# Optimization experiments

Measured on AMD Instinct MI355X. Metric: run time of the kernel, lower is better.

## Reference

```python
import jax, jax.numpy as jnp
import numpy as np

N_EMBD = 1024
N_HEAD = 16
HEAD_SIZE = 64


def setup_inputs() -> dict:
    key = jax.random.key(0)
    ks = jax.random.split(key, 6)
    B, T, C, H, D = 2, 2048, N_EMBD, N_HEAD, HEAD_SIZE
    s = 1.0 / np.sqrt(C)
    x = jax.random.normal(ks[0], (B, T, C), dtype=jnp.float32)
    Wq = jax.random.normal(ks[1], (H, C, D), dtype=jnp.float32) * s
    Wk = jax.random.normal(ks[2], (H, C, D), dtype=jnp.float32) * s
    Wv = jax.random.normal(ks[3], (H, C, D), dtype=jnp.float32) * s
    Wo = jax.random.normal(ks[4], (H * D, C), dtype=jnp.float32) * (1.0 / np.sqrt(H * D))
    bo = jax.random.normal(ks[5], (C,), dtype=jnp.float32) * 0.01
    return {"x": x, "Wq": Wq, "Wk": Wk, "Wv": Wv, "Wo": Wo, "bo": bo}


def reference(x, Wq, Wk, Wv, Wo, bo):
    B, T, C = x.shape
    H, _, D = Wq.shape
    # Per-head projections, batched across heads: [B,H,T,D]
    q = jnp.einsum('btc,hcd->bhtd', x, Wq)
    k = jnp.einsum('btc,hcd->bhtd', x, Wk)
    v = jnp.einsum('btc,hcd->bhtd', x, Wv)
    # NOTE: original scales by sqrt(C) = sqrt(n_embd), not sqrt(head_size)
    scale = 1.0 / jnp.sqrt(jnp.float32(C))
    att = jnp.einsum('bhtd,bhsd->bhts', q, k) * scale  # [B,H,T,T]
    causal = jnp.tril(jnp.ones((T, T), dtype=bool))
    att = jnp.where(causal, att, -jnp.inf)
    att = jax.nn.softmax(att, axis=-1)
    # dropout omitted (eval mode / deterministic reference)
    out = jnp.einsum('bhts,bhsd->bhtd', att, v)  # [B,H,T,D]
    out = out.transpose(0, 2, 1, 3).reshape(B, T, H * D)
    return out @ Wo + bo
```

## Files before the change

kernel.cpp:

```cpp
#include <hip/hip_runtime.h>
#include <hip/hip_bf16.h>


typedef __hip_bfloat16 bf16;
typedef __bf16 v8bf __attribute__((ext_vector_type(8)));
typedef float  v4f  __attribute__((ext_vector_type(4)));
typedef unsigned long long u64;
typedef unsigned int u32;

#define MFMA16(a, b, c) __builtin_amdgcn_mfma_f32_16x16x32_bf16((a), (b), (c), 0, 0, 0)

__device__ __forceinline__ bf16 f2b(float x) { return __float2bfloat16(x); }
__device__ __forceinline__ __bf16 f2braw(float x) {
  bf16 t = __float2bfloat16(x);
  return *reinterpret_cast<__bf16*>(&t);
}
__device__ __forceinline__ unsigned short f2bu(float x) {
  bf16 t = __float2bfloat16(x);
  return *reinterpret_cast<unsigned short*>(&t);
}

__device__ __forceinline__ void load16_lds(const bf16* gptr, const bf16* lptr) {
  __builtin_amdgcn_global_load_lds(
      (const __attribute__((address_space(1))) u32*)gptr,
      (__attribute__((address_space(3))) u32*)lptr, 16, 0, 0);
}

__global__ __launch_bounds__(256) void prep_kernel(
    const float* __restrict__ x,
    const float* __restrict__ Wq, const float* __restrict__ Wk,
    const float* __restrict__ Wv, const float* __restrict__ Wo,
    bf16* __restrict__ xb, bf16* __restrict__ wt, bf16* __restrict__ wot)
{
  __shared__ float Lt[32][33];
  const int bid = blockIdx.x, tid = threadIdx.x;

  if (bid < 2048) {
    size_t i = ((size_t)bid * 256 + tid) * 8;
    float4 f0 = *(const float4*)(x + i);
    float4 f1 = *(const float4*)(x + i + 4);
    v8bf v;
    v[0] = f2braw(f0.x); v[1] = f2braw(f0.y); v[2] = f2braw(f0.z); v[3] = f2braw(f0.w);
    v[4] = f2braw(f1.x); v[5] = f2braw(f1.y); v[6] = f2braw(f1.z); v[7] = f2braw(f1.w);
    *(v8bf*)(xb + i) = v;
    return;
  }
  const int tx = tid & 31, ty = tid >> 5;
  if (bid < 5120) {
    const int idx = bid - 2048;
    const int z = idx >> 6, rem = idx & 63;
    const int p = z >> 4, h = z & 15;
    const float* ib = ((p == 0) ? Wq : (p == 1) ? Wk : Wv) + (size_t)h * 65536;
    bf16* ob = wt + (size_t)z * 65536;
    const int j0 = (rem & 1) * 32, i0 = (rem >> 1) * 32;
    #pragma unroll
    for (int r = 0; r < 4; ++r)
      Lt[ty + 8 * r][tx] = ib[(size_t)(i0 + ty + 8 * r) * 64 + j0 + tx];
    __syncthreads();
    #pragma unroll
    for (int r = 0; r < 4; ++r)
      ob[(size_t)(j0 + ty + 8 * r) * 1024 + i0 + tx] = f2b(Lt[tx][ty + 8 * r]);
  } else {
    const int idx = bid - 5120;
    const int j0 = (idx & 31) * 32, i0 = (idx >> 5) * 32;
    #pragma unroll
    for (int r = 0; r < 4; ++r)
      Lt[ty + 8 * r][tx] = Wo[(size_t)(i0 + ty + 8 * r) * 1024 + j0 + tx];
    __syncthreads();
    #pragma unroll
    for (int r = 0; r < 4; ++r)
      wot[(size_t)(j0 + ty + 8 * r) * 1024 + i0 + tx] = f2b(Lt[tx][ty + 8 * r]);
  }
}

__global__ __launch_bounds__(512, 2) void qkv_gemm_kernel(
    const bf16* __restrict__ xb, const bf16* __restrict__ wt,
    bf16* __restrict__ qkv)
{
  __shared__ __align__(16) bf16 Ash[2][256][64];
  __shared__ __align__(16) bf16 Bsh[2][192][64];

  const int mt = blockIdx.x, nt = blockIdx.y;
  const int tid = threadIdx.x, wid = tid >> 6, lane = tid & 63;
  const int ln = lane & 15, quad = lane >> 4;
  const int wm = wid >> 1, wn = wid & 1;
  const int m0 = mt * 256, n0 = nt * 192;

  const v4f vzero = {0.f, 0.f, 0.f, 0.f};
  v4f acc[4][6];
  #pragma unroll
  for (int mf = 0; mf < 4; ++mf)
    #pragma unroll
    for (int nf = 0; nf < 6; ++nf) acc[mf][nf] = vzero;

  const int r8 = lane >> 3, slot = (lane & 7) ^ r8;
  const bf16* gA0 = xb + (size_t)(m0 + (wid * 4 + 0) * 8 + r8) * 1024 + slot * 8;
  const bf16* gA1 = xb + (size_t)(m0 + (wid * 4 + 1) * 8 + r8) * 1024 + slot * 8;
  const bf16* gA2 = xb + (size_t)(m0 + (wid * 4 + 2) * 8 + r8) * 1024 + slot * 8;
  const bf16* gA3 = xb + (size_t)(m0 + (wid * 4 + 3) * 8 + r8) * 1024 + slot * 8;
  const bf16* gB0 = wt + (size_t)(n0 + (wid * 3 + 0) * 8 + r8) * 1024 + slot * 8;
  const bf16* gB1 = wt + (size_t)(n0 + (wid * 3 + 1) * 8 + r8) * 1024 + slot * 8;
  const bf16* gB2 = wt + (size_t)(n0 + (wid * 3 + 2) * 8 + r8) * 1024 + slot * 8;

  const int sw = ln & 7;
  const int fs0 = ((quad    ) ^ sw) * 8;
  const int fs1 = ((quad + 4) ^ sw) * 8;
  const int arow = (wm * 64 + ln) * 64;
  const int brow = (wn * 96 + ln) * 64;

  #define STAGE_A(BUF) {                                         \
    load16_lds(gA0, &Ash[BUF][(wid * 4 + 0) * 8][0]);            \
    load16_lds(gA1, &Ash[BUF][(wid * 4 + 1) * 8][0]);            \
    load16_lds(gA2, &Ash[BUF][(wid * 4 + 2) * 8][0]);            \
    load16_lds(gA3, &Ash[BUF][(wid * 4 + 3) * 8][0]);            \
    gA0 += 64; gA1 += 64; gA2 += 64; gA3 += 64; }
  #define STAGE_B(BUF) {                                         \
    load16_lds(gB0, &Bsh[BUF][(wid * 3 + 0) * 8][0]);            \
    load16_lds(gB1, &Bsh[BUF][(wid * 3 + 1) * 8][0]);            \
    load16_lds(gB2, &Bsh[BUF][(wid * 3 + 2) * 8][0]);            \
    gB0 += 64; gB1 += 64; gB2 += 64; }

  #define PHASE_SYNC() {                                         \
    __builtin_amdgcn_s_barrier();                                \
    asm volatile("s_waitcnt lgkmcnt(0)" ::: "memory");           \
    __builtin_amdgcn_sched_barrier(0); }

  #define QTILE(BUF, DOSTAGE, DOBOUND)                                     \
  {                                                                        \
    const bf16* aB = &Ash[BUF][0][0];                                      \
    const bf16* bB = &Bsh[BUF][0][0];                                      \
    v8bf af[4], bv[3];                                                     \
                              \
    _Pragma("unroll")                                                      \
    for (int mf = 0; mf < 4; ++mf)                                         \
      af[mf] = *(const v8bf*)(aB + arow + mf * 1024 + fs0);                \
    _Pragma("unroll")                                                      \
    for (int nf = 0; nf < 3; ++nf)                                         \
      bv[nf] = *(const v8bf*)(bB + brow + nf * 1024 + fs0);                \
    if (DOSTAGE) STAGE_A(BUF ^ 1)                                          \
    PHASE_SYNC()                                                           \
    __builtin_amdgcn_s_setprio(1);                                         \
    _Pragma("unroll")                                                      \
    for (int mf = 0; mf < 4; ++mf)                                         \
      _Pragma("unroll")                                                    \
      for (int nf = 0; nf < 3; ++nf)                                       \
        acc[mf][nf] = MFMA16(af[mf], bv[nf], acc[mf][nf]);                 \
    __builtin_amdgcn_s_setprio(0);                                         \
                                        \
    _Pragma("unroll")                                                      \
    for (int nf = 0; nf < 3; ++nf)                                         \
      bv[nf] = *(const v8bf*)(bB + brow + (nf + 3) * 1024 + fs0);          \
    if (DOSTAGE) STAGE_B(BUF ^ 1)                                          \
    PHASE_SYNC()                                                           \
    __builtin_amdgcn_s_setprio(1);                                         \
    _Pragma("unroll")                                                      \
    for (int mf = 0; mf < 4; ++mf)                                         \
      _Pragma("unroll")                                                    \
      for (int nf = 0; nf < 3; ++nf)                                       \
        acc[mf][nf + 3] = MFMA16(af[mf], bv[nf], acc[mf][nf + 3]);         \
    __builtin_amdgcn_s_setprio(0);                                         \
                                            \
    _Pragma("unroll")                                                      \
    for (int mf = 0; mf < 4; ++mf)                                         \
      af[mf] = *(const v8bf*)(aB + arow + mf * 1024 + fs1);                \
    _Pragma("unroll")                                                      \
    for (int nf = 0; nf < 3; ++nf)                                         \
      bv[nf] = *(const v8bf*)(bB + brow + nf * 1024 + fs1);                \
    PHASE_SYNC()                                                           \
    __builtin_amdgcn_s_setprio(1);                                         \
    _Pragma("unroll")                                                      \
    for (int mf = 0; mf < 4; ++mf)                                         \
      _Pragma("unroll")                                                    \
      for (int nf = 0; nf < 3; ++nf)                                       \
        acc[mf][nf] = MFMA16(af[mf], bv[nf], acc[mf][nf]);                 \
    __builtin_amdgcn_s_setprio(0);                                         \
                                                      \
    _Pragma("unroll")                                                      \
    for (int nf = 0; nf < 3; ++nf)                                         \
      bv[nf] = *(const v8bf*)(bB + brow + (nf + 3) * 1024 + fs1);          \
    PHASE_SYNC()                                                           \
    __builtin_amdgcn_s_setprio(1);                                         \
    _Pragma("unroll")                                                      \
    for (int mf = 0; mf < 4; ++mf)                                         \
      _Pragma("unroll")                                                    \
      for (int nf = 0; nf < 3; ++nf)                                       \
        acc[mf][nf + 3] = MFMA16(af[mf], bv[nf], acc[mf][nf + 3]);         \
    __builtin_amdgcn_s_setprio(0);                                         \
        \
    if (DOBOUND) {                                                         \
      asm volatile("s_waitcnt vmcnt(0) lgkmcnt(0)" ::: "memory");          \
      __builtin_amdgcn_s_barrier();                                        \
      __builtin_amdgcn_sched_barrier(0);                                   \
    }                                                                      \
  }

  STAGE_A(0)
  STAGE_B(0)
  asm volatile("s_waitcnt vmcnt(0)" ::: "memory");
  __builtin_amdgcn_s_barrier();
  __builtin_amdgcn_sched_barrier(0);

  #pragma unroll 1
  for (int it = 0; it < 7; ++it) {
    QTILE(0, 1, 1)
    QTILE(1, 1, 1)
  }
  QTILE(0, 1, 1)
  QTILE(1, 0, 0)
  #undef QTILE
  #undef PHASE_SYNC
  #undef STAGE_A
  #undef STAGE_B

  #pragma unroll
  for (int nf = 0; nf < 6; ++nf) {
    const int j = n0 + wn * 96 + nf * 16 + ln;
    const int p = j >> 10;
    const int h = (j >> 6) & 15;
    const int d = j & 63;
    if (p < 2) {
      const float scale = (p == 0) ? 0.0450841149f : 1.0f;
      bf16* base = qkv + (size_t)p * 4194304 + (size_t)h * 262144;
      #pragma unroll
      for (int mf = 0; mf < 4; ++mf)
        #pragma unroll
        for (int r = 0; r < 4; ++r) {
          int m = m0 + wm * 64 + mf * 16 + quad * 4 + r;
          base[(size_t)m * 64 + d] = f2b(acc[mf][nf][r] * scale);
        }
    } else {
      bf16* vb = qkv + (size_t)2 * 4194304 + (size_t)h * 262144;
      #pragma unroll
      for (int mf = 0; mf < 4; ++mf) {
        int mrow = m0 + wm * 64 + mf * 16 + quad * 4;
        int bi = mrow >> 11, t0 = mrow & 2047;
        u64 pk = (u64)f2bu(acc[mf][nf][0]) |
                 ((u64)f2bu(acc[mf][nf][1]) << 16) |
                 ((u64)f2bu(acc[mf][nf][2]) << 32) |
                 ((u64)f2bu(acc[mf][nf][3]) << 48);
        *(u64*)(vb + (size_t)bi * 131072 + (size_t)d * 2048 + t0) = pk;
      }
    }
  }
}

__global__ __launch_bounds__(256, 4) void attn_kernel(
    const bf16* __restrict__ qkv, bf16* __restrict__ att)
{
  union ShU {
    struct { bf16 K[2][64][64]; bf16 V[2][64][64]; } t;
    struct { float O[2][64][36]; float L[2][36]; } c;
  };
  __shared__ __align__(16) ShU sh;

  const int fid = blockIdx.x;
  const int j = fid >> 5;
  const int jr = j & 7, jq = j >> 3;
  const int mt = (jq == 0) ? (31 - jr) : (jq == 1) ? (8 + jr)
               : (jq == 2) ? (23 - jr) : jr;
  const int grp = fid & 31;
  const int b = grp >> 4, h = grp & 15;

  const int tid = threadIdx.x, w = tid >> 6, lane = tid & 63;
  const int ln = lane & 15, quad = lane >> 4;
  const int qh = w & 1, kh = w >> 1;

  const bf16* qbase  = qkv + (size_t)h * 262144 + (size_t)b * 131072;
  const bf16* kbase  = qbase + 4194304;
  const bf16* vtbase = qbase + 8388608;

  const int l8 = lane & 7, r8 = lane >> 3;
  const int slot = l8 ^ r8;
  const int p0 = w * 16 + r8, p1 = p0 + 8;
  const int kp0 = (p0 & 32) | ((p0 & 12) << 1) | ((p0 & 16) >> 2) | (p0 & 3);
  const int kp1 = (p1 & 32) | ((p1 & 12) << 1) | ((p1 & 16) >> 2) | (p1 & 3);
  const bf16* gkp0 = kbase + kp0 * 64 + slot * 8;
  const bf16* gkp1 = kbase + kp1 * 64 + slot * 8;
  const bf16* gvp0 = vtbase + p0 * 2048 + slot * 8;
  const bf16* gvp1 = gvp0 + 8 * 2048;

  const int sw = ln & 7;
  const int cc0 = ((quad    ) ^ sw) * 8;
  const int cc1 = ((quad + 4) ^ sw) * 8;
  const int cck = kh ? cc1 : cc0;
  const int krow0 = (kh * 32 + ln) * 64;
  const int ka0 = krow0 + cc0, ka1 = krow0 + cc1;
  const int voff = ln * 64 + cck;

  v8bf vone;
  {
    unsigned short u = 0x3F80;
    __bf16 e = *reinterpret_cast<__bf16*>(&u);
    #pragma unroll
    for (int jj = 0; jj < 8; ++jj) vone[jj] = e;
  }
  const v4f vzero = {0.f, 0.f, 0.f, 0.f};
  const float NEG = -30000.0f;

  #define STAGE2(BUF) {                                          \
    load16_lds(gkp0, &sh.t.K[BUF][w * 16][0]);                   \
    load16_lds(gkp1, &sh.t.K[BUF][w * 16 + 8][0]);               \
    load16_lds(gvp0, &sh.t.V[BUF][w * 16][0]);                   \
    load16_lds(gvp1, &sh.t.V[BUF][w * 16 + 8][0]);               \
    gkp0 += 4096; gkp1 += 4096; gvp0 += 64; gvp1 += 64; }

  const int row0 = mt * 64;
  const int qrow = row0 + qh * 32;

  v8bf aq[2][2];
  #pragma unroll
  for (int mc = 0; mc < 2; ++mc)
    #pragma unroll
    for (int ks = 0; ks < 2; ++ks)
      aq[mc][ks] = *(const v8bf*)(qbase +
          (size_t)(qrow + mc * 16 + ln) * 64 + ks * 32 + quad * 8);

  v4f o[2][4], lacc[2];
  #pragma unroll
  for (int mc = 0; mc < 2; ++mc) {
    lacc[mc] = vzero;
    #pragma unroll
    for (int dt = 0; dt < 4; ++dt) o[mc][dt] = vzero;
  }

  const int kb_end = mt;
  int kb = 0;
  STAGE2(0)

  #define TILE(BUF)                                                        \
  {                                                                        \
    __syncthreads();                                    \
    const bf16* krB = &sh.t.K[BUF][0][0];                                  \
    const bf16* vrB = &sh.t.V[BUF][0][0];                                  \
    v8bf kf[2][2], vf[4];                                                  \
    kf[0][0] = *(const v8bf*)(krB + ka0);                                  \
    kf[1][0] = *(const v8bf*)(krB + ka1);                                  \
    kf[0][1] = *(const v8bf*)(krB + ka0 + 1024);                           \
    kf[1][1] = *(const v8bf*)(krB + ka1 + 1024);                           \
    vf[0] = *(const v8bf*)(vrB + voff);                                    \
    vf[1] = *(const v8bf*)(vrB + voff + 1024);                             \
    vf[2] = *(const v8bf*)(vrB + voff + 2048);                             \
    vf[3] = *(const v8bf*)(vrB + voff + 3072);                             \
    if (kb < kb_end) STAGE2(BUF ^ 1)                                       \
    _Pragma("unroll")                                                      \
    for (int mc = 0; mc < 2; ++mc) {                                       \
      __builtin_amdgcn_s_setprio(1);                                       \
      v4f s[2];                                                            \
      s[0] = vzero; s[1] = vzero;                                          \
      _Pragma("unroll")                                                    \
      for (int ks = 0; ks < 2; ++ks) {                                     \
        s[0] = MFMA16(kf[ks][0], aq[mc][ks], s[0]);                        \
        s[1] = MFMA16(kf[ks][1], aq[mc][ks], s[1]);                        \
      }                                                                    \
      __builtin_amdgcn_s_setprio(0);                                       \
      const int qg = qrow + mc * 16 + ln;                                  \
      if (kb == kb_end) {                      \
        _Pragma("unroll")                                                  \
        for (int nfl = 0; nfl < 2; ++nfl) {                                \
          const int kc = kb * 64 + kh * 32 + quad * 8 + nfl * 4;           \
          _Pragma("unroll")                                                \
          for (int r = 0; r < 4; ++r)                                      \
            if (kc + r > qg) s[nfl][r] = NEG;                              \
        }                                                                  \
      }                                                                    \
      float ex[2][4];                                                      \
      _Pragma("unroll")                                                    \
      for (int nfl = 0; nfl < 2; ++nfl)                                    \
        _Pragma("unroll")                                                  \
        for (int r = 0; r < 4; ++r)                                        \
          ex[nfl][r] = exp2f(s[nfl][r]);                                   \
      union { u32 uw[4]; v8bf v; } pu;                                     \
      _Pragma("unroll")                                                    \
      for (int nfl = 0; nfl < 2; ++nfl)                                    \
        _Pragma("unroll")                                                  \
        for (int wi = 0; wi < 2; ++wi)                                     \
          asm("v_cvt_pk_bf16_f32 %0, %1, %2"                               \
              : "=v"(pu.uw[nfl * 2 + wi])                                  \
              : "v"(ex[nfl][2 * wi]), "v"(ex[nfl][2 * wi + 1]));           \
      __builtin_amdgcn_s_setprio(1);                                       \
      lacc[mc] = MFMA16(pu.v, vone, lacc[mc]);                             \
      _Pragma("unroll")                                                    \
      for (int dt = 0; dt < 4; ++dt)                                       \
        o[mc][dt] = MFMA16(pu.v, vf[dt], o[mc][dt]);                       \
      __builtin_amdgcn_s_setprio(0);                                       \
    }                                                                      \
  }

  while (true) {
    TILE(0)
    if (kb >= kb_end) break;
    ++kb;
    TILE(1)
    if (kb >= kb_end) break;
    ++kb;
  }
  #undef TILE
  #undef STAGE2

  __syncthreads();
  if (kh == 1) {
    #pragma unroll
    for (int mc = 0; mc < 2; ++mc) {
      #pragma unroll
      for (int dt = 0; dt < 4; ++dt)
        *(v4f*)&sh.c.O[qh][dt * 16 + ln][mc * 16 + quad * 4] = o[mc][dt];
      if (ln == 0)
        *(v4f*)&sh.c.L[qh][mc * 16 + quad * 4] = lacc[mc];
    }
  }
  __syncthreads();
  if (kh == 0) {
    #pragma unroll
    for (int mc = 0; mc < 2; ++mc) {
      v4f pl = *(const v4f*)&sh.c.L[qh][mc * 16 + quad * 4];
      v4f inv;
      #pragma unroll
      for (int r = 0; r < 4; ++r) inv[r] = 1.0f / (lacc[mc][r] + pl[r]);
      #pragma unroll
      for (int dt = 0; dt < 4; ++dt) {
        v4f po = *(const v4f*)&sh.c.O[qh][dt * 16 + ln][mc * 16 + quad * 4];
        #pragma unroll
        for (int r = 0; r < 4; ++r) {
          int m = b * 2048 + qrow + mc * 16 + quad * 4 + r;
          att[(size_t)m * 1024 + h * 64 + dt * 16 + ln] =
              f2b((o[mc][dt][r] + po[r]) * inv[r]);
        }
      }
    }
  }
}

__global__ __launch_bounds__(256) void out_gemm_kernel(
    const bf16* __restrict__ att, const bf16* __restrict__ wot,
    const float* __restrict__ bo, float* __restrict__ out)
{
  __shared__ __align__(16) bf16 Ash[3][128][32];
  __shared__ __align__(16) bf16 Bsh[3][64][32];

  const int mt = blockIdx.x, nt = blockIdx.y;
  const int tid = threadIdx.x, w = tid >> 6, lane = tid & 63;
  const int ln = lane & 15, quad = lane >> 4;
  const int wm = w >> 1, wn = w & 1;
  const int m0 = mt * 128, n0 = nt * 64;

  const v4f vzero = {0.f, 0.f, 0.f, 0.f};
  v4f acc[4][2];
  #pragma unroll
  for (int mf = 0; mf < 4; ++mf)
    #pragma unroll
    for (int nf = 0; nf < 2; ++nf) acc[mf][nf] = vzero;

  const int srow = lane >> 2;
  const int sseg = ((lane & 3) ^ ((lane >> 3) & 3)) * 8;
  const bf16* ga = att + (size_t)(m0 + 32 * w + srow) * 1024 + sseg;
  const bf16* gb = wot + (size_t)(n0 + 16 * w + srow) * 1024 + sseg;

  const int fseg = (quad ^ ((ln >> 1) & 3)) * 8;

  #define OSTAGE(BUF) {                                          \
    load16_lds(ga,             &Ash[BUF][32 * w][0]);            \
    load16_lds(ga + 16 * 1024, &Ash[BUF][32 * w + 16][0]);       \
    load16_lds(gb,             &Bsh[BUF][16 * w][0]);            \
    ga += 32; gb += 32; }

  OSTAGE(0)
  OSTAGE(1)

  #define OSTEP(BUF, VM, DOSTAGE)                                          \
  {                                                                        \
    asm volatile("s_waitcnt vmcnt(" #VM ") lgkmcnt(0)" ::: "memory");      \
    __builtin_amdgcn_s_barrier();                                          \
    __builtin_amdgcn_sched_barrier(0);                                     \
    v8bf af[4], bfv[2];                                                    \
    _Pragma("unroll")                                                      \
    for (int mf = 0; mf < 4; ++mf)                                         \
      af[mf] = *(const v8bf*)&Ash[BUF][wm * 64 + mf * 16 + ln][fseg];      \
    _Pragma("unroll")                                                      \
    for (int nf = 0; nf < 2; ++nf)                                         \
      bfv[nf] = *(const v8bf*)&Bsh[BUF][wn * 32 + nf * 16 + ln][fseg];     \
    if (DOSTAGE) OSTAGE((BUF + 2) % 3)                                     \
    __builtin_amdgcn_s_setprio(1);                                         \
    _Pragma("unroll")                                                      \
    for (int mf = 0; mf < 4; ++mf)                                         \
      _Pragma("unroll")                                                    \
      for (int nf = 0; nf < 2; ++nf)                                       \
        acc[mf][nf] = MFMA16(af[mf], bfv[nf], acc[mf][nf]);                \
    __builtin_amdgcn_s_setprio(0);                                         \
  }

  #pragma unroll 1
  for (int it = 0; it < 10; ++it) {
    OSTEP(0, 3, 1)
    OSTEP(1, 3, 1)
    OSTEP(2, 3, 1)
  }
  OSTEP(0, 3, 0)
  OSTEP(1, 0, 0)
  #undef OSTEP
  #undef OSTAGE

  #pragma unroll
  for (int nf = 0; nf < 2; ++nf) {
    int j = n0 + wn * 32 + nf * 16 + ln;
    float bias = bo[j];
    #pragma unroll
    for (int mf = 0; mf < 4; ++mf)
      #pragma unroll
      for (int r = 0; r < 4; ++r) {
        int m = m0 + wm * 64 + mf * 16 + quad * 4 + r;
        out[(size_t)m * 1024 + j] = acc[mf][nf][r] + bias;
      }
  }
}

extern "C" void kernel_launch(void* const* d_in, const int* in_sizes, int n_in,
                              void* d_out, int out_size, void* d_ws, size_t ws_size,
                              hipStream_t stream) {
  const float* x  = (const float*)d_in[0];
  const float* Wq = (const float*)d_in[1];
  const float* Wk = (const float*)d_in[2];
  const float* Wv = (const float*)d_in[3];
  const float* Wo = (const float*)d_in[4];
  const float* bo = (const float*)d_in[5];
  float* out = (float*)d_out;

  bf16* xb  = (bf16*)d_ws;
  bf16* wt  = xb + 4194304;
  bf16* wot = xb + 7340032;
  bf16* qkv = xb + 8388608;
  bf16* att = xb + 20971520;

  prep_kernel<<<6144, 256, 0, stream>>>(x, Wq, Wk, Wv, Wo, xb, wt, wot);
  qkv_gemm_kernel<<<dim3(16, 16), 512, 0, stream>>>(xb, wt, qkv);
  attn_kernel<<<1024, 256, 0, stream>>>(qkv, att);
  out_gemm_kernel<<<dim3(32, 16), 256, 0, stream>>>(att, wot, bo, out);
}
```

Before: 163.3 us.

## Restructure output GEMM to double-buffered 64-wide K tiles with phased staging

The output projection GEMM moves from a triple-buffered 32-wide K pipeline to a double-buffered 64-wide K tile with an XOR swizzle. Each tile is processed in two phases whose global-to-LDS loads are interleaved between MFMA groups, mirroring the QKV kernel's schedule. This halves the number of K iterations and barriers per tile step and widens the loads. The cost is one fewer buffer of prefetch depth and a full drain at each tile boundary.

```diff
diff --git a/kernel.cpp b/kernel.cpp
--- a/kernel.cpp
+++ b/kernel.cpp
@@ -130,7 +130,6 @@
     const bf16* aB = &Ash[BUF][0][0];                                      \
     const bf16* bB = &Bsh[BUF][0][0];                                      \
     v8bf af[4], bv[3];                                                     \
-                              \
     _Pragma("unroll")                                                      \
     for (int mf = 0; mf < 4; ++mf)                                         \
       af[mf] = *(const v8bf*)(aB + arow + mf * 1024 + fs0);                \
@@ -146,7 +145,6 @@
       for (int nf = 0; nf < 3; ++nf)                                       \
         acc[mf][nf] = MFMA16(af[mf], bv[nf], acc[mf][nf]);                 \
     __builtin_amdgcn_s_setprio(0);                                         \
-                                        \
     _Pragma("unroll")                                                      \
     for (int nf = 0; nf < 3; ++nf)                                         \
       bv[nf] = *(const v8bf*)(bB + brow + (nf + 3) * 1024 + fs0);          \
@@ -159,7 +157,6 @@
       for (int nf = 0; nf < 3; ++nf)                                       \
         acc[mf][nf + 3] = MFMA16(af[mf], bv[nf], acc[mf][nf + 3]);         \
     __builtin_amdgcn_s_setprio(0);                                         \
-                                            \
     _Pragma("unroll")                                                      \
     for (int mf = 0; mf < 4; ++mf)                                         \
       af[mf] = *(const v8bf*)(aB + arow + mf * 1024 + fs1);                \
@@ -174,7 +171,6 @@
       for (int nf = 0; nf < 3; ++nf)                                       \
         acc[mf][nf] = MFMA16(af[mf], bv[nf], acc[mf][nf]);                 \
     __builtin_amdgcn_s_setprio(0);                                         \
-                                                      \
     _Pragma("unroll")                                                      \
     for (int nf = 0; nf < 3; ++nf)                                         \
       bv[nf] = *(const v8bf*)(bB + brow + (nf + 3) * 1024 + fs1);          \
@@ -186,7 +182,6 @@
       for (int nf = 0; nf < 3; ++nf)                                       \
         acc[mf][nf + 3] = MFMA16(af[mf], bv[nf], acc[mf][nf + 3]);         \
     __builtin_amdgcn_s_setprio(0);                                         \
-        \
     if (DOBOUND) {                                                         \
       asm volatile("s_waitcnt vmcnt(0) lgkmcnt(0)" ::: "memory");          \
       __builtin_amdgcn_s_barrier();                                        \
@@ -434,8 +429,8 @@
     const bf16* __restrict__ att, const bf16* __restrict__ wot,
     const float* __restrict__ bo, float* __restrict__ out)
 {
-  __shared__ __align__(16) bf16 Ash[3][128][32];
-  __shared__ __align__(16) bf16 Bsh[3][64][32];
+  __shared__ __align__(16) bf16 Ash[2][128][64];
+  __shared__ __align__(16) bf16 Bsh[2][64][64];
 
   const int mt = blockIdx.x, nt = blockIdx.y;
   const int tid = threadIdx.x, w = tid >> 6, lane = tid & 63;
@@ -450,54 +445,98 @@
     #pragma unroll
     for (int nf = 0; nf < 2; ++nf) acc[mf][nf] = vzero;
 
-  const int srow = lane >> 2;
-  const int sseg = ((lane & 3) ^ ((lane >> 3) & 3)) * 8;
-  const bf16* ga = att + (size_t)(m0 + 32 * w + srow) * 1024 + sseg;
-  const bf16* gb = wot + (size_t)(n0 + 16 * w + srow) * 1024 + sseg;
-
-  const int fseg = (quad ^ ((ln >> 1) & 3)) * 8;
-
-  #define OSTAGE(BUF) {                                          \
-    load16_lds(ga,             &Ash[BUF][32 * w][0]);            \
-    load16_lds(ga + 16 * 1024, &Ash[BUF][32 * w + 16][0]);       \
-    load16_lds(gb,             &Bsh[BUF][16 * w][0]);            \
-    ga += 32; gb += 32; }
-
-  OSTAGE(0)
-  OSTAGE(1)
-
-  #define OSTEP(BUF, VM, DOSTAGE)                                          \
+  const int r8 = lane >> 3, slot = (lane & 7) ^ r8;
+  const bf16* gA0 = att + (size_t)(m0 + (w * 4 + 0) * 8 + r8) * 1024 + slot * 8;
+  const bf16* gA1 = att + (size_t)(m0 + (w * 4 + 1) * 8 + r8) * 1024 + slot * 8;
+  const bf16* gA2 = att + (size_t)(m0 + (w * 4 + 2) * 8 + r8) * 1024 + slot * 8;
+  const bf16* gA3 = att + (size_t)(m0 + (w * 4 + 3) * 8 + r8) * 1024 + slot * 8;
+  const bf16* gB0 = wot + (size_t)(n0 + (w * 2 + 0) * 8 + r8) * 1024 + slot * 8;
+  const bf16* gB1 = wot + (size_t)(n0 + (w * 2 + 1) * 8 + r8) * 1024 + slot * 8;
+
+  const int sw = ln & 7;
+  const int fs0 = ((quad    ) ^ sw) * 8;
+  const int fs1 = ((quad + 4) ^ sw) * 8;
+  const int arow = (wm * 64 + ln) * 64;
+  const int brow = (wn * 32 + ln) * 64;
+
+  #define OSTAGE_A1(BUF) {                                       \
+    load16_lds(gA0, &Ash[BUF][(w * 4 + 0) * 8][0]);              \
+    load16_lds(gA1, &Ash[BUF][(w * 4 + 1) * 8][0]);              \
+    gA0 += 64; gA1 += 64; }
+  #define OSTAGE_A2B(BUF) {                                      \
+    load16_lds(gA2, &Ash[BUF][(w * 4 + 2) * 8][0]);              \
+    load16_lds(gA3, &Ash[BUF][(w * 4 + 3) * 8][0]);              \
+    load16_lds(gB0, &Bsh[BUF][(w * 2 + 0) * 8][0]);              \
+    load16_lds(gB1, &Bsh[BUF][(w * 2 + 1) * 8][0]);              \
+    gA2 += 64; gA3 += 64; gB0 += 64; gB1 += 64; }
+
+  #define OPHASE_SYNC() {                                        \
+    __builtin_amdgcn_s_barrier();                                \
+    asm volatile("s_waitcnt lgkmcnt(0)" ::: "memory");           \
+    __builtin_amdgcn_sched_barrier(0); }
+
+  #define OTILE(BUF, DOSTAGE, DOBOUND)                                     \
   {                                                                        \
-    asm volatile("s_waitcnt vmcnt(" #VM ") lgkmcnt(0)" ::: "memory");      \
-    __builtin_amdgcn_s_barrier();                                          \
-    __builtin_amdgcn_sched_barrier(0);                                     \
-    v8bf af[4], bfv[2];                                                    \
-    _Pragma("unroll")                                                      \
-    for (int mf = 0; mf < 4; ++mf)                                         \
-      af[mf] = *(const v8bf*)&Ash[BUF][wm * 64 + mf * 16 + ln][fseg];      \
+    const bf16* aB = &Ash[BUF][0][0];                                      \
+    const bf16* bB = &Bsh[BUF][0][0];                                      \
+    v8bf af[4], bv[2];                                                     \
+                                     \
+    _Pragma("unroll")                                                      \
+    for (int mf = 0; mf < 4; ++mf)                                         \
+      af[mf] = *(const v8bf*)(aB + arow + mf * 1024 + fs0);                \
     _Pragma("unroll")                                                      \
     for (int nf = 0; nf < 2; ++nf)                                         \
-      bfv[nf] = *(const v8bf*)&Bsh[BUF][wn * 32 + nf * 16 + ln][fseg];     \
-    if (DOSTAGE) OSTAGE((BUF + 2) % 3)                                     \
+      bv[nf] = *(const v8bf*)(bB + brow + nf * 1024 + fs0);                \
+    if (DOSTAGE) OSTAGE_A1(BUF ^ 1)                                        \
+    OPHASE_SYNC()                                                          \
     __builtin_amdgcn_s_setprio(1);                                         \
     _Pragma("unroll")                                                      \
     for (int mf = 0; mf < 4; ++mf)                                         \
       _Pragma("unroll")                                                    \
       for (int nf = 0; nf < 2; ++nf)                                       \
-        acc[mf][nf] = MFMA16(af[mf], bfv[nf], acc[mf][nf]);                \
+        acc[mf][nf] = MFMA16(af[mf], bv[nf], acc[mf][nf]);                 \
     __builtin_amdgcn_s_setprio(0);                                         \
-  }
+                                 \
+    _Pragma("unroll")                                                      \
+    for (int mf = 0; mf < 4; ++mf)                                         \
+      af[mf] = *(const v8bf*)(aB + arow + mf * 1024 + fs1);                \
+    _Pragma("unroll")                                                      \
+    for (int nf = 0; nf < 2; ++nf)                                         \
+      bv[nf] = *(const v8bf*)(bB + brow + nf * 1024 + fs1);                \
+    if (DOSTAGE) OSTAGE_A2B(BUF ^ 1)                                       \
+    OPHASE_SYNC()                                                          \
+    __builtin_amdgcn_s_setprio(1);                                         \
+    _Pragma("unroll")                                                      \
+    for (int mf = 0; mf < 4; ++mf)                                         \
+      _Pragma("unroll")                                                    \
+      for (int nf = 0; nf < 2; ++nf)                                       \
+        acc[mf][nf] = MFMA16(af[mf], bv[nf], acc[mf][nf]);                 \
+    __builtin_amdgcn_s_setprio(0);                                         \
+                         \
+    if (DOBOUND) {                                                         \
+      asm volatile("s_waitcnt vmcnt(0) lgkmcnt(0)" ::: "memory");          \
+      __builtin_amdgcn_s_barrier();                                        \
+      __builtin_amdgcn_sched_barrier(0);                                   \
+    }                                                                      \
+  }
+
+  OSTAGE_A1(0)
+  OSTAGE_A2B(0)
+  asm volatile("s_waitcnt vmcnt(0)" ::: "memory");
+  __builtin_amdgcn_s_barrier();
+  __builtin_amdgcn_sched_barrier(0);
 
   #pragma unroll 1
-  for (int it = 0; it < 10; ++it) {
-    OSTEP(0, 3, 1)
-    OSTEP(1, 3, 1)
-    OSTEP(2, 3, 1)
-  }
-  OSTEP(0, 3, 0)
-  OSTEP(1, 0, 0)
-  #undef OSTEP
-  #undef OSTAGE
+  for (int it = 0; it < 7; ++it) {
+    OTILE(0, 1, 1)
+    OTILE(1, 1, 1)
+  }
+  OTILE(0, 1, 1)
+  OTILE(1, 0, 0)
+  #undef OTILE
+  #undef OPHASE_SYNC
+  #undef OSTAGE_A1
+  #undef OSTAGE_A2B
 
   #pragma unroll
   for (int nf = 0; nf < 2; ++nf) {
```

After: 165.3 us. No clear change (+1.2%).
